# Performance work log

Measured on AMD Instinct MI355X. Metric: run time of the kernel, lower is better.

## Reference

```python
import math
import jax, jax.numpy as jnp
import numpy as np

B, T, C = 2, 768, 64
N_HEAD = 64
HEAD_DIM = C // N_HEAD  # = 1 (forced by the Kronecker-lift shape constraint)


def _alibi_slopes(n_heads):
    def pow2_slopes(n):
        start = 2 ** (-2 ** (-(math.log2(n) - 3)))
        return [start * (start ** i) for i in range(n)]
    if math.log2(n_heads).is_integer():
        s = pow2_slopes(n_heads)
    else:
        closest = 2 ** math.floor(math.log2(n_heads))
        s = pow2_slopes(closest)
        s.extend(pow2_slopes(2 * closest)[0::2][: n_heads - closest])
    return np.asarray(s, dtype=np.float32)


def _kron_block_apply(z, tmp):
    """Apply M.T where M = block_diag_h(kron(eye(hd), tmp[h])). z:(B,T,C), tmp:(H,hd,hd).
    Per head-block, for z reshaped (a,d) over (hd,hd): out[a,c] = sum_d tmp[h,c,d] * z[a,d]."""
    Bz, Tz, Cz = z.shape
    H, hd, _ = tmp.shape
    zr = z.reshape(Bz, Tz, H, hd, hd)
    return jnp.einsum('bthad,hcd->bthac', zr, tmp).reshape(Bz, Tz, Cz)


def setup_inputs() -> dict:
    key = jax.random.key(0)
    kx, kw, kv, kp = jax.random.split(key, 4)
    x = jax.random.normal(kx, (B, T, C), dtype=jnp.float32)
    W_attn = jax.random.normal(kw, (2 * C, C), dtype=jnp.float32) * 0.02
    v_tmp = jax.random.normal(kv, (N_HEAD, HEAD_DIM, HEAD_DIM), dtype=jnp.float32)
    proj_tmp = jax.random.normal(kp, (N_HEAD, HEAD_DIM, HEAD_DIM), dtype=jnp.float32)
    return {"x": x, "W_attn": W_attn, "v_tmp": v_tmp, "proj_tmp": proj_tmp}


def reference(x, W_attn, v_tmp, proj_tmp):
    Bx, Tx, Cx = x.shape
    H = v_tmp.shape[0]
    head_dim = Cx // H
    # q, k projection (use_v=True -> c_attn maps C -> 2C, no bias)
    qk = x @ W_attn.T
    q, k = jnp.split(qk, 2, axis=-1)
    # Kronecker-lifted V transform (block-diagonal structure applied directly)
    v = _kron_block_apply(x, v_tmp)
    # (B,T,H,d) -> (B,H,T,d)
    q = q.reshape(Bx, Tx, H, head_dim).transpose(0, 2, 1, 3)
    k = k.reshape(Bx, Tx, H, head_dim).transpose(0, 2, 1, 3)
    v = v.reshape(Bx, Tx, H, head_dim).transpose(0, 2, 1, 3)
    scale = 1.0 / math.sqrt(head_dim)
    scores = jnp.einsum('bhid,bhjd->bhij', q, k) * scale
    # ALiBi bias: positions clamped at 0 (NOTE: source has no causal -inf mask)
    pos = jnp.minimum(jnp.arange(Tx)[None, :] - jnp.arange(Tx)[:, None], 0).astype(x.dtype)
    slopes = jnp.asarray(_alibi_slopes(H), dtype=x.dtype)
    scores = scores + slopes[None, :, None, None] * pos[None, None, :, :]
    w = jax.nn.softmax(scores, axis=-1)
    y = jnp.einsum('bhij,bhjd->bhid', w, v)
    y = y.transpose(0, 2, 1, 3).reshape(Bx, Tx, Cx)
    # Kronecker-lifted output projection
    y = _kron_block_apply(y, proj_tmp)
    return y
```

## Files before the change

kernel.cpp:

```cpp
#include <hip/hip_runtime.h>
#include <stdint.h>

constexpr int Tc = 768;
constexpr int Hc = 64;
constexpr int Bc = 2;
constexpr float LOG2E = 1.44269504088896f;
constexpr size_t SLAB = (size_t)Bc * Hc * Tc;

typedef float v4f __attribute__((ext_vector_type(4)));

__global__ __launch_bounds__(256) void proj_kernel(
    const float* __restrict__ x, const float* __restrict__ W,
    const float* __restrict__ vtmp, const float* __restrict__ ptmp,
    float* __restrict__ qs, float* __restrict__ ks, float* __restrict__ vs)
{
    const int lane = threadIdx.x & 63;
    const int w    = __builtin_amdgcn_readfirstlane(threadIdx.x >> 6);
    const int g    = blockIdx.x * 64 + lane;
    const int bh0  = (g / Tc) * Hc;
    const int t    = g % Tc;
    const int h    = blockIdx.y * 4 + w;

    float xr[64];
    const v4f* xp = (const v4f*)(x + (size_t)g * 64);
#pragma unroll
    for (int c = 0; c < 16; ++c) ((v4f*)xr)[c] = xp[c];

    const float* __restrict__ wq = W + h * 64;
    const float* __restrict__ wk = W + (64 + h) * 64;
    float aq = 0.f, ak = 0.f;
#pragma unroll
    for (int c = 0; c < 64; ++c) {
        aq = fmaf(xr[c], wq[c], aq);
        ak = fmaf(xr[c], wk[c], ak);
    }
    const size_t o = (size_t)(bh0 + h) * Tc + t;
    qs[o] = aq * LOG2E;
    ks[o] = ak;
    vs[o] = x[(size_t)g * 64 + h] * vtmp[h] * ptmp[h];
}

__device__ __forceinline__ float dpp_reduce_add(float v) {
    v += __int_as_float(__builtin_amdgcn_update_dpp(0, __float_as_int(v), 0x111, 0xf, 0xf, true));
    v += __int_as_float(__builtin_amdgcn_update_dpp(0, __float_as_int(v), 0x112, 0xf, 0xf, true));
    v += __int_as_float(__builtin_amdgcn_update_dpp(0, __float_as_int(v), 0x114, 0xf, 0xf, true));
    v += __int_as_float(__builtin_amdgcn_update_dpp(0, __float_as_int(v), 0x118, 0xf, 0xf, true));
    v += __int_as_float(__builtin_amdgcn_update_dpp(0, __float_as_int(v), 0x142, 0xf, 0xf, true));
    v += __int_as_float(__builtin_amdgcn_update_dpp(0, __float_as_int(v), 0x143, 0xf, 0xf, true));
    return v;
}

__global__ __launch_bounds__(256, 6) void attn_kernel(
    const float* __restrict__ qs, const float* __restrict__ ks,
    const float* __restrict__ vs, float* __restrict__ out)
{
    const int lane = threadIdx.x & 63;
    const int w    = __builtin_amdgcn_readfirstlane(threadIdx.x >> 6);
    const int rt   = blockIdx.x;
    const int h    = blockIdx.y;
    const int b    = blockIdx.z;
    const int bh   = b * Hc + h;

    const float slope2 = exp2f(-0.125f * (float)(h + 1)) * LOG2E;

    const float* __restrict__ kp = ks + (size_t)bh * Tc;
    const float* __restrict__ vp = vs + (size_t)bh * Tc;
    const float* __restrict__ qp = qs + (size_t)bh * Tc;

    float kr[12], vr[12], bj[12];
#pragma unroll
    for (int r = 0; r < 12; ++r) {
        const int j = lane + 64 * r;
        kr[r] = kp[j];
        vr[r] = vp[j];
        bj[r] = slope2 * (float)j;
    }

    const int i0 = rt * 64 + w * 16;
    float si = slope2 * (float)i0;
#pragma unroll 2
    for (int ii = 0; ii < 16; ++ii) {
        const int i  = i0 + ii;
        const float q = qp[i];
        float sum = 0.f, acc = 0.f;
#pragma unroll
        for (int r = 0; r < 12; ++r) {
            float d = fminf(bj[r] - si, 0.f);
            float e = __builtin_amdgcn_exp2f(fmaf(q, kr[r], d));
            sum += e;
            acc  = fmaf(e, vr[r], acc);
        }
        sum = dpp_reduce_add(sum);
        acc = dpp_reduce_add(acc);
        if (lane == 63) {
            out[((size_t)(b * Tc + i)) * 64 + h] = acc * __builtin_amdgcn_rcpf(sum);
        }
        si += slope2;
    }
}

extern "C" void kernel_launch(void* const* d_in, const int* in_sizes, int n_in,
                              void* d_out, int out_size, void* d_ws, size_t ws_size,
                              hipStream_t stream) {
    const float* x    = (const float*)d_in[0];
    const float* W    = (const float*)d_in[1];
    const float* vtmp = (const float*)d_in[2];
    const float* ptmp = (const float*)d_in[3];
    float* out = (float*)d_out;

    float* qsl = (float*)d_ws;
    float* ksl = qsl + SLAB;
    float* vsl = ksl + SLAB;

    proj_kernel<<<dim3(24, 16), 256, 0, stream>>>(x, W, vtmp, ptmp, qsl, ksl, vsl);
    attn_kernel<<<dim3(12, Hc, Bc), 256, 0, stream>>>(qsl, ksl, vsl, out);
}
```

Measured before the change: 80.92 us.

## Map query rows to lanes and stage K/V in LDS instead of cross-lane reductions

The attention kernel now gives each lane its own query row and splits the key range across the four waves. K and V are staged interleaved in shared memory and read as broadcast loads. This removes the per-row DPP wave reductions and the single-lane stores in favour of one small LDS reduction across waves at the end. The cost is LDS traffic, two block barriers, and uniform LDS reads on every inner iteration.

```diff
diff --git a/kernel.cpp b/kernel.cpp
--- a/kernel.cpp
+++ b/kernel.cpp
@@ -7,6 +7,7 @@
 constexpr float LOG2E = 1.44269504088896f;
 constexpr size_t SLAB = (size_t)Bc * Hc * Tc;
 
+typedef float v2f __attribute__((ext_vector_type(2)));
 typedef float v4f __attribute__((ext_vector_type(4)));
 
 __global__ __launch_bounds__(256) void proj_kernel(
@@ -40,62 +41,64 @@
     vs[o] = x[(size_t)g * 64 + h] * vtmp[h] * ptmp[h];
 }
 
-__device__ __forceinline__ float dpp_reduce_add(float v) {
-    v += __int_as_float(__builtin_amdgcn_update_dpp(0, __float_as_int(v), 0x111, 0xf, 0xf, true));
-    v += __int_as_float(__builtin_amdgcn_update_dpp(0, __float_as_int(v), 0x112, 0xf, 0xf, true));
-    v += __int_as_float(__builtin_amdgcn_update_dpp(0, __float_as_int(v), 0x114, 0xf, 0xf, true));
-    v += __int_as_float(__builtin_amdgcn_update_dpp(0, __float_as_int(v), 0x118, 0xf, 0xf, true));
-    v += __int_as_float(__builtin_amdgcn_update_dpp(0, __float_as_int(v), 0x142, 0xf, 0xf, true));
-    v += __int_as_float(__builtin_amdgcn_update_dpp(0, __float_as_int(v), 0x143, 0xf, 0xf, true));
-    return v;
-}
-
 __global__ __launch_bounds__(256, 6) void attn_kernel(
     const float* __restrict__ qs, const float* __restrict__ ks,
     const float* __restrict__ vs, float* __restrict__ out)
 {
-    const int lane = threadIdx.x & 63;
-    const int w    = __builtin_amdgcn_readfirstlane(threadIdx.x >> 6);
+    const int tid  = threadIdx.x;
+    const int lane = tid & 63;
+    const int w    = __builtin_amdgcn_readfirstlane(tid >> 6);
     const int rt   = blockIdx.x;
     const int h    = blockIdx.y;
     const int b    = blockIdx.z;
     const int bh   = b * Hc + h;
 
-    const float slope2 = exp2f(-0.125f * (float)(h + 1)) * LOG2E;
+    __shared__ v2f  kv[Tc];
+    __shared__ float psum[4][64], pacc[4][64];
 
     const float* __restrict__ kp = ks + (size_t)bh * Tc;
     const float* __restrict__ vp = vs + (size_t)bh * Tc;
-    const float* __restrict__ qp = qs + (size_t)bh * Tc;
 
-    float kr[12], vr[12], bj[12];
 #pragma unroll
-    for (int r = 0; r < 12; ++r) {
-        const int j = lane + 64 * r;
-        kr[r] = kp[j];
-        vr[r] = vp[j];
-        bj[r] = slope2 * (float)j;
+    for (int r = 0; r < 3; ++r) {
+        const int t = tid + 256 * r;
+        v2f e; e.x = kp[t]; e.y = vp[t];
+        kv[t] = e;
     }
 
-    const int i0 = rt * 64 + w * 16;
-    float si = slope2 * (float)i0;
-#pragma unroll 2
-    for (int ii = 0; ii < 16; ++ii) {
-        const int i  = i0 + ii;
-        const float q = qp[i];
-        float sum = 0.f, acc = 0.f;
+    const int i = rt * 64 + lane;
+    const float q = qs[(size_t)bh * Tc + i];
+    const float slope2 = exp2f(-0.125f * (float)(h + 1)) * LOG2E;
+
+    float cu[16];
 #pragma unroll
-        for (int r = 0; r < 12; ++r) {
-            float d = fminf(bj[r] - si, 0.f);
-            float e = __builtin_amdgcn_exp2f(fmaf(q, kr[r], d));
+    for (int u = 0; u < 16; ++u) cu[u] = slope2 * (float)u;
+
+    __syncthreads();
+
+    const int j0 = w * (Tc / 4);
+    const v2f* __restrict__ kvq = &kv[j0];
+    float sum = 0.f, acc = 0.f;
+    for (int c = 0; c < 12; ++c) {
+        const float mb = slope2 * (float)(j0 + 16 * c - i);
+#pragma unroll
+        for (int u = 0; u < 16; ++u) {
+            v2f kvj = kvq[16 * c + u];
+            float d = fminf(mb + cu[u], 0.f);
+            float e = __builtin_amdgcn_exp2f(fmaf(q, kvj.x, d));
             sum += e;
-            acc  = fmaf(e, vr[r], acc);
+            acc  = fmaf(e, kvj.y, acc);
         }
-        sum = dpp_reduce_add(sum);
-        acc = dpp_reduce_add(acc);
-        if (lane == 63) {
-            out[((size_t)(b * Tc + i)) * 64 + h] = acc * __builtin_amdgcn_rcpf(sum);
-        }
-        si += slope2;
+    }
+    psum[w][lane] = sum;
+    pacc[w][lane] = acc;
+    __syncthreads();
+
+    if (tid < 64) {
+        float s = psum[0][lane] + psum[1][lane] + psum[2][lane] + psum[3][lane];
+        float a = pacc[0][lane] + pacc[1][lane] + pacc[2][lane] + pacc[3][lane];
+        out[((size_t)(b * Tc + rt * 64 + lane)) * 64 + h] =
+            a * __builtin_amdgcn_rcpf(s);
     }
 }
 
```

After: 78.19 us. 1.03x faster.
